# Kernel tuning notes

Measured on AMD Instinct MI355X. Metric: run time of the kernel, lower is better.

## Reference

```python
import jax, jax.numpy as jnp
import numpy as np

N_NODES = 50000
N_EDGES = 500000
N_REL = 8
D = 128        # input_dim
A_DIM = 64     # attention_dim
D_OUT = 128    # output_dim


def setup_inputs() -> dict:
    key = jax.random.key(0)
    ks = jax.random.split(key, 10)
    h = jax.random.normal(ks[0], (N_NODES, D), jnp.float32)
    # relation gate tables: [R, 2*D, D]; first D rows act on dst (subject), last D on src (object)
    relations = jax.random.normal(ks[1], (N_REL, 2 * D, D), jnp.float32) * 0.05
    rel_attention = jax.random.normal(ks[2], (N_REL, A_DIM), jnp.float32) * 0.05
    W_a = jax.random.normal(ks[3], (A_DIM, 2 * D), jnp.float32) * 0.05
    b_a = jnp.zeros((A_DIM,), jnp.float32)
    W_lin = jax.random.normal(ks[4], (D_OUT, 2 * D), jnp.float32) * 0.05
    b_lin = jnp.zeros((D_OUT,), jnp.float32)
    src = jax.random.randint(ks[5], (N_EDGES,), 0, N_NODES, dtype=jnp.int32)
    dst = jax.random.randint(ks[6], (N_EDGES,), 0, N_NODES, dtype=jnp.int32)
    etype = jax.random.randint(ks[7], (N_EDGES,), 0, N_REL, dtype=jnp.int32)
    return {"h": h, "relations": relations, "rel_attention": rel_attention,
            "W_a": W_a, "b_a": b_a, "W_lin": W_lin, "b_lin": b_lin,
            "src": src, "dst": dst, "etype": etype}


def reference(h, relations, rel_attention, W_a, b_a, W_lin, b_lin, src, dst, etype):
    d = h.shape[-1]
    # --- gates: relation-indexed gather_mm (concat gate type) ---
    # Project every node through every relation once (R is small), then gather per edge.
    proj_dst = jnp.einsum('nd,rde->rne', h, relations[:, :d, :])   # [R, N, D] subject/dst side
    proj_src = jnp.einsum('nd,rde->rne', h, relations[:, d:, :])   # [R, N, D] object/src side
    gate = jax.nn.sigmoid(proj_dst[etype, dst] + proj_src[etype, src])  # [E, D]

    src_h = h[src]   # [E, D]
    dst_h = h[dst]   # [E, D]

    # --- gatv2 attention (predicates are zeroed in the module -> rel_attention[0]) ---
    a = jax.nn.leaky_relu(jnp.concatenate([dst_h, src_h], axis=-1) @ W_a.T + b_a)  # [E, A]
    score = (rel_attention[0] * a).sum(-1)  # [E]

    # --- edge_softmax over destination-node segments ---
    smax = jax.ops.segment_max(score, dst, num_segments=N_NODES)
    ex = jnp.exp(score - smax[dst])
    denom = jax.ops.segment_sum(ex, dst, num_segments=N_NODES)
    attn = ex / denom[dst]  # [E]

    # --- message = u_mul_e(h, attn*gate), reduce = sum over dst ---
    msg = src_h * (attn[:, None] * gate)                 # [E, D]
    h_N = jax.ops.segment_sum(msg, dst, num_segments=N_NODES)  # [N, D]

    # --- graphsage aggregate: LeakyReLU(W [h ; h_N] + b) ---
    out = jax.nn.leaky_relu(jnp.concatenate([h, h_N], axis=-1) @ W_lin.T + b_lin)
    return out
```

## Files before the change

### kernel.cpp

```cpp
#include <hip/hip_runtime.h>
#include <cstdint>
#include <cstddef>

constexpr int NNODES = 50000;
constexpr int NEDGES = 500000;
constexpr int NRELS  = 8;
constexpr int DIM    = 128;
constexpr int ADIM   = 64;
constexpr int TWOD   = 256;
constexpr int EPB    = 64;
constexpr float SLOPE = 0.01f;

constexpr int XPITCH = TWOD + 8;
constexpr int SPAD = NEDGES + 1024;
constexpr int SCAN_CHUNK = 1000;
constexpr int NB_SCAN = NRELS * NNODES / SCAN_CHUNK;

typedef __attribute__((ext_vector_type(8))) short short8;
typedef __attribute__((ext_vector_type(4))) float floatx4;

__device__ __forceinline__ unsigned short f2bf(float f) {
    unsigned u = __float_as_uint(f);
    unsigned r = u + 0x7FFFu + ((u >> 16) & 1u);
    return (unsigned short)(r >> 16);
}
__device__ __forceinline__ float bf2f(unsigned short b) {
    return __uint_as_float(((unsigned)b) << 16);
}
__device__ __forceinline__ float sigmoid_fast(float x) {
    return __builtin_amdgcn_rcpf(1.0f + __expf(-x));
}

__global__ void k_init(int* __restrict__ histD, int* __restrict__ histRD,
                       int* __restrict__ cursorRD) {
    int i = blockIdx.x * blockDim.x + threadIdx.x;
    int stride = gridDim.x * blockDim.x;
    for (int idx = i; idx < NNODES; idx += stride) histD[idx] = 0;
    for (int idx = i; idx < NRELS * NNODES; idx += stride) {
        histRD[idx] = 0;
        cursorRD[idx] = 0;
    }
}

__global__ __launch_bounds__(256) void k_prep(const float* __restrict__ rel,
                                              const float* __restrict__ W_lin,
                                              const float* __restrict__ W_a,
                                              unsigned short* __restrict__ relT,
                                              unsigned short* __restrict__ Wl,
                                              unsigned short* __restrict__ Wa16) {
    __shared__ float ls[64][65];
    int b = blockIdx.x, t = threadIdx.x;
    if (b < 64) {
        int r = b >> 3, tile = b & 7;
        int d0 = (tile >> 1) * 64, o0 = (tile & 1) * 64;
        const float* rp = rel + ((size_t)r * TWOD + d0) * DIM + o0;
#pragma unroll
        for (int u = 0; u < 16; u++) {
            int v = u * 256 + t;
            int j = v & 63, i = v >> 6;
            ls[i][j] = rp[(size_t)i * DIM + j];
        }
        __syncthreads();
        unsigned short* wp = relT + ((size_t)r * DIM + o0) * TWOD + d0;
#pragma unroll
        for (int u = 0; u < 16; u++) {
            int v = u * 256 + t;
            int ii = v & 63, jj = v >> 6;
            wp[(size_t)jj * TWOD + ii] = f2bf(ls[ii][jj]);
        }
    } else {
        int idx = (b - 64) * 256 + t;
        if (idx < DIM * TWOD) {
            Wl[idx] = f2bf(W_lin[idx]);
        } else {
            int j = idx - DIM * TWOD;
            if (j < ADIM * TWOD) Wa16[j] = f2bf(W_a[j]);
        }
    }
}

__global__ void k_h16(const float* __restrict__ h, unsigned short* __restrict__ h16) {
    int i = blockIdx.x * 256 + threadIdx.x;
    if (i < NNODES * DIM / 8) {
        const float4* hp = (const float4*)(h + (size_t)i * 8);
        float4 a = hp[0], b = hp[1];
        union { unsigned short us[8]; short8 s8; } pk;
        pk.us[0] = f2bf(a.x); pk.us[1] = f2bf(a.y); pk.us[2] = f2bf(a.z); pk.us[3] = f2bf(a.w);
        pk.us[4] = f2bf(b.x); pk.us[5] = f2bf(b.y); pk.us[6] = f2bf(b.z); pk.us[7] = f2bf(b.w);
        *(short8*)&h16[(size_t)i * 8] = pk.s8;
    }
}

__global__ void k_hist2(const int* __restrict__ ety, const int* __restrict__ dst,
                        int* __restrict__ histRD, int* __restrict__ histD) {
    int e = blockIdx.x * 256 + threadIdx.x;
    if (e < NEDGES) {
        int r = ety[e], dn = dst[e];
        atomicAdd(&histRD[r * NNODES + dn], 1);
        atomicAdd(&histD[dn], 1);
    }
}

__global__ __launch_bounds__(256) void k_scanA(int* __restrict__ histRD,
                                               int* __restrict__ blockSums) {
    __shared__ int part[256];
    int b = blockIdx.x, t = threadIdx.x;
    int base = b * SCAN_CHUNK;
    int i0 = t * 4;
    int v[4]; int s = 0;
#pragma unroll
    for (int j = 0; j < 4; j++) {
        int i = i0 + j;
        v[j] = (i < SCAN_CHUNK) ? histRD[base + i] : 0;
        s += v[j];
    }
    part[t] = s;
    __syncthreads();
    for (int off = 1; off < 256; off <<= 1) {
        int x = (t >= off) ? part[t - off] : 0;
        __syncthreads();
        part[t] += x;
        __syncthreads();
    }
    int run = (t == 0) ? 0 : part[t - 1];
#pragma unroll
    for (int j = 0; j < 4; j++) {
        int i = i0 + j;
        if (i < SCAN_CHUNK) { histRD[base + i] = run; run += v[j]; }
    }
    if (t == 255) blockSums[b] = part[255];
}

__global__ __launch_bounds__(1024) void k_scanB(const int* __restrict__ blockSums,
                                                int* __restrict__ bp2,
                                                const int* __restrict__ histD,
                                                int* __restrict__ row_ptr,
                                                int* __restrict__ cursorD,
                                                int* __restrict__ offs,
                                                uint2* __restrict__ sMeta) {
    __shared__ int ls[1024];
    __shared__ int s_offs[NRELS + 1];
    __shared__ int s_cnt[NRELS];
    __shared__ int s_adj[NRELS];
    const int t = threadIdx.x;

    ls[t] = (t < NB_SCAN) ? blockSums[t] : 0;
    __syncthreads();
    for (int off = 1; off < 1024; off <<= 1) {
        int v = (t >= off) ? ls[t - off] : 0;
        __syncthreads();
        ls[t] += v;
        __syncthreads();
    }
    if (t == 0) {
        const int BPB = NNODES / SCAN_CHUNK;
        int off = 0;
        for (int r = 0; r < NRELS; r++) {
            int sf0 = (r == 0) ? 0 : ls[BPB * r - 1];
            int sf1 = ls[BPB * (r + 1) - 1];
            int cnt = sf1 - sf0;
            offs[r] = off; s_offs[r] = off; s_cnt[r] = cnt;
            s_adj[r] = off - sf0;
            off += ((cnt + EPB - 1) / EPB) * EPB;
        }
        s_offs[NRELS] = off;
    }
    __syncthreads();
    if (t < NB_SCAN) {
        int sf = (t == 0) ? 0 : ls[t - 1];
        bp2[t] = sf + s_adj[t / (NNODES / SCAN_CHUNK)];
    }
    __syncthreads();

    const int CH = (NNODES + 1023) / 1024;
    const int base = t * CH;
    int s = 0;
    for (int j = 0; j < CH; j++) { int i = base + j; if (i < NNODES) s += histD[i]; }
    ls[t] = s;
    __syncthreads();
    for (int off = 1; off < 1024; off <<= 1) {
        int v = (t >= off) ? ls[t - off] : 0;
        __syncthreads();
        ls[t] += v;
        __syncthreads();
    }
    int run = (t == 0) ? 0 : ls[t - 1];
    for (int j = 0; j < CH; j++) {
        int i = base + j;
        if (i < NNODES) { row_ptr[i] = run; cursorD[i] = 0; run += histD[i]; }
    }
    if (t == 1023) row_ptr[NNODES] = ls[1023];
    __syncthreads();

#pragma unroll
    for (int r = 0; r < NRELS; r++) {
        int s0 = s_offs[r] + s_cnt[r];
        int e0 = s_offs[r + 1];
        for (int idx = s0 + t; idx < e0; idx += 1024) sMeta[idx] = make_uint2(0xFFFFFFFFu, 0u);
    }
    for (int idx = s_offs[NRELS] + t; idx < SPAD; idx += 1024)
        sMeta[idx] = make_uint2(0xFFFFFFFFu, 0u);
}

__global__ void k_escatter(const int* __restrict__ ety, const int* __restrict__ src,
                           const int* __restrict__ dst, const int* __restrict__ row_ptr,
                           const int* __restrict__ histRD, const int* __restrict__ bp2,
                           int* __restrict__ cursorRD, int* __restrict__ cursorD,
                           uint2* __restrict__ sMeta) {
    int e = blockIdx.x * 256 + threadIdx.x;
    if (e >= NEDGES) return;
    int r = ety[e], sn = src[e], dn = dst[e];
    int idx = r * NNODES + dn;
    int rank = atomicAdd(&cursorRD[idx], 1);
    int slot = histRD[idx] + bp2[idx / SCAN_CHUNK] + rank;
    int pos = row_ptr[dn] + atomicAdd(&cursorD[dn], 1);
    sMeta[slot] = make_uint2((unsigned)sn | ((unsigned)dn << 16), (unsigned)pos);
}

__global__ __launch_bounds__(256, 4) void k_gate_msg(
    const unsigned short* __restrict__ h16, const unsigned short* __restrict__ relT,
    const unsigned short* __restrict__ Wa16,
    const uint2* __restrict__ sMeta, const float* __restrict__ b_a,
    const float* __restrict__ ratt, const int* __restrict__ offs,
    unsigned short* __restrict__ msgbuf, float* __restrict__ scoreP) {
    __shared__ unsigned short Xs[EPB * XPITCH];
    __shared__ int srcn_s[EPB];
    __shared__ int dstn_s[EPB];
    __shared__ int pos_s[EPB];
    __shared__ int val_s[EPB];
    __shared__ float scoreW[EPB][4];

    const int t = threadIdx.x;
    const int base = blockIdx.x * EPB;

    if (t < EPB) {
        uint2 m2 = sMeta[base + t];
        int valid = (m2.x != 0xFFFFFFFFu);
        val_s[t] = valid;
        srcn_s[t] = valid ? (int)(m2.x & 0xFFFFu) : 0;
        dstn_s[t] = valid ? (int)(m2.x >> 16) : 0;
        pos_s[t] = valid ? (int)m2.y : 0;
    }
    __syncthreads();
    if (!val_s[0]) return;

    int r = 0;
#pragma unroll
    for (int i = 1; i < NRELS; i++) if (base >= offs[i]) r = i;

#pragma unroll
    for (int u = 0; u < 8; u++) {
        int v = u * 256 + t;
        int i = v >> 5;
        int c = v & 31;
        int node = (c < 16) ? dstn_s[i] : srcn_s[i];
        *(short8*)&Xs[i * XPITCH + c * 8] = *(const short8*)&h16[(size_t)node * DIM + (c & 15) * 8];
    }

    const int wave = t >> 6;
    const int lane = t & 63;
    const int q = lane >> 4;
    const int l16 = lane & 15;
    const int o16 = wave * 16 + l16;

    const unsigned short* bp0 = relT + ((size_t)r * DIM + (wave * 2 + 0) * 16 + l16) * TWOD + q * 8;
    const unsigned short* bp1 = relT + ((size_t)r * DIM + (wave * 2 + 1) * 16 + l16) * TWOD + q * 8;
    const unsigned short* wb  = Wa16 + (size_t)o16 * TWOD + q * 8;

    short8 B0p[4], B1p[4], BSp[4];
#pragma unroll
    for (int ks = 0; ks < 4; ks++) {
        B0p[ks] = *(const short8*)(bp0 + ks * 32);
        B1p[ks] = *(const short8*)(bp1 + ks * 32);
        BSp[ks] = *(const short8*)(wb + ks * 32);
    }

    __syncthreads();

    floatx4 acc[4][2];
    floatx4 accS[4];
#pragma unroll
    for (int m = 0; m < 4; m++) {
        acc[m][0] = (floatx4)(0.0f);
        acc[m][1] = (floatx4)(0.0f);
        accS[m] = (floatx4)(0.0f);
    }

#pragma unroll
    for (int ks = 0; ks < 8; ks++) {
        short8 B0 = (ks < 4) ? B0p[ks & 3] : *(const short8*)(bp0 + ks * 32);
        short8 B1 = (ks < 4) ? B1p[ks & 3] : *(const short8*)(bp1 + ks * 32);
        short8 BS = (ks < 4) ? BSp[ks & 3] : *(const short8*)(wb + ks * 32);
        short8 Af[4];
        const unsigned short* xb = &Xs[l16 * XPITCH + ks * 32 + q * 8];
#pragma unroll
        for (int m = 0; m < 4; m++) Af[m] = *(const short8*)(xb + m * 16 * XPITCH);
#pragma unroll
        for (int m = 0; m < 4; m++) {
            acc[m][0] = __builtin_amdgcn_mfma_f32_16x16x32_bf16(Af[m], B0, acc[m][0], 0, 0, 0);
            acc[m][1] = __builtin_amdgcn_mfma_f32_16x16x32_bf16(Af[m], B1, acc[m][1], 0, 0, 0);
            accS[m]   = __builtin_amdgcn_mfma_f32_16x16x32_bf16(Af[m], BS, accS[m], 0, 0, 0);
        }
    }

    __syncthreads();

    {
        float ba = b_a[o16];
        float ra = ratt[o16];
#pragma unroll
        for (int m = 0; m < 4; m++) {
#pragma unroll
            for (int rg = 0; rg < 4; rg++) {
                float v = accS[m][rg] + ba;
                v = v > 0.0f ? v : SLOPE * v;
                v *= ra;
#pragma unroll
                for (int off = 8; off > 0; off >>= 1) v += __shfl_xor(v, off, 16);
                if (l16 == 0) scoreW[m * 16 + q * 4 + rg][wave] = v;
            }
        }
    }

#pragma unroll
    for (int m = 0; m < 4; m++) {
        int ib = m * 16 + q * 4;
#pragma unroll
        for (int nn = 0; nn < 2; nn++) {
            int o = (wave * 2 + nn) * 16 + l16;
#pragma unroll
            for (int rg = 0; rg < 4; rg++) {
                int i = ib + rg;
                float g = sigmoid_fast(acc[m][nn][rg]);
                float sh = bf2f(Xs[i * XPITCH + DIM + o]);
                Xs[i * XPITCH + o] = f2bf(sh * g);
            }
        }
    }
    __syncthreads();

#pragma unroll
    for (int u = 0; u < 4; u++) {
        int v = u * 256 + t;
        int i = v >> 4;
        int c = v & 15;
        if (!val_s[i]) continue;
        short8 val = *(const short8*)&Xs[i * XPITCH + c * 8];
        *(short8*)&msgbuf[(size_t)pos_s[i] * DIM + c * 8] = val;
    }
    if (t < EPB && val_s[t]) {
        scoreP[pos_s[t]] = scoreW[t][0] + scoreW[t][1] + scoreW[t][2] + scoreW[t][3];
    }
}

__global__ __launch_bounds__(256) void k_aggr(const unsigned short* __restrict__ msgbuf,
                                              const float* __restrict__ scoreP,
                                              const int* __restrict__ row_ptr,
                                              unsigned short* __restrict__ hN16) {
    int n = blockIdx.x * 4 + (threadIdx.x >> 6);
    int lane = threadIdx.x & 63;
    if (n >= NNODES) return;
    int p0 = row_ptr[n], p1 = row_ptr[n + 1];
    float a0 = 0.0f, a1 = 0.0f;
    if (p0 < p1) {
        float mx = -3.0e38f;
        for (int p = p0 + lane; p < p1; p += 64) mx = fmaxf(mx, scoreP[p]);
#pragma unroll
        for (int off = 32; off > 0; off >>= 1) mx = fmaxf(mx, __shfl_xor(mx, off));
        float sum = 0.0f;
        for (int p = p0 + lane; p < p1; p += 64) sum += __expf(scoreP[p] - mx);
#pragma unroll
        for (int off = 32; off > 0; off >>= 1) sum += __shfl_xor(sum, off);
        int p = p0;
        const unsigned short* mb = msgbuf + (size_t)lane * 2;
        for (; p + 4 <= p1; p += 4) {
            float w0 = __expf(scoreP[p + 0] - mx);
            float w1 = __expf(scoreP[p + 1] - mx);
            float w2 = __expf(scoreP[p + 2] - mx);
            float w3 = __expf(scoreP[p + 3] - mx);
            unsigned v0 = *(const unsigned*)&mb[(size_t)(p + 0) * DIM];
            unsigned v1 = *(const unsigned*)&mb[(size_t)(p + 1) * DIM];
            unsigned v2 = *(const unsigned*)&mb[(size_t)(p + 2) * DIM];
            unsigned v3 = *(const unsigned*)&mb[(size_t)(p + 3) * DIM];
            a0 = fmaf(w0, bf2f((unsigned short)(v0 & 0xFFFFu)), a0);
            a1 = fmaf(w0, bf2f((unsigned short)(v0 >> 16)), a1);
            a0 = fmaf(w1, bf2f((unsigned short)(v1 & 0xFFFFu)), a0);
            a1 = fmaf(w1, bf2f((unsigned short)(v1 >> 16)), a1);
            a0 = fmaf(w2, bf2f((unsigned short)(v2 & 0xFFFFu)), a0);
            a1 = fmaf(w2, bf2f((unsigned short)(v2 >> 16)), a1);
            a0 = fmaf(w3, bf2f((unsigned short)(v3 & 0xFFFFu)), a0);
            a1 = fmaf(w3, bf2f((unsigned short)(v3 >> 16)), a1);
        }
        for (; p < p1; p++) {
            float w = __expf(scoreP[p] - mx);
            unsigned v = *(const unsigned*)&mb[(size_t)p * DIM];
            a0 = fmaf(w, bf2f((unsigned short)(v & 0xFFFFu)), a0);
            a1 = fmaf(w, bf2f((unsigned short)(v >> 16)), a1);
        }
        float inv = __builtin_amdgcn_rcpf(sum);
        a0 *= inv; a1 *= inv;
    }
    unsigned o = (unsigned)f2bf(a0) | ((unsigned)f2bf(a1) << 16);
    *(unsigned*)&hN16[(size_t)n * DIM + lane * 2] = o;
}

__global__ __launch_bounds__(256) void k_out(const unsigned short* __restrict__ h16,
                                             const unsigned short* __restrict__ hN16,
                                             const unsigned short* __restrict__ Wl,
                                             const float* __restrict__ b_lin,
                                             float* __restrict__ out) {
    __shared__ unsigned short Xs[EPB * XPITCH];
    const int t = threadIdx.x;
    const int nb = blockIdx.x * 64;

#pragma unroll
    for (int u = 0; u < 8; u++) {
        int v = u * 256 + t;
        int i = v >> 5;
        int c = v & 31;
        int n = nb + i;
        if (n >= NNODES) n = NNODES - 1;
        const unsigned short* srcp = (c < 16) ? h16 : hN16;
        *(short8*)&Xs[i * XPITCH + c * 8] = *(const short8*)&srcp[(size_t)n * DIM + (c & 15) * 8];
    }

    const int wave = t >> 6;
    const int lane = t & 63;
    const int q = lane >> 4;
    const int l16 = lane & 15;

    short8 Bf[2][8];
#pragma unroll
    for (int nn = 0; nn < 2; nn++) {
        int o = (wave * 2 + nn) * 16 + l16;
        const unsigned short* bp = Wl + (size_t)o * TWOD + q * 8;
#pragma unroll
        for (int ks = 0; ks < 8; ks++) Bf[nn][ks] = *(const short8*)(bp + ks * 32);
    }

    __syncthreads();

    floatx4 acc[4][2];
#pragma unroll
    for (int m = 0; m < 4; m++)
#pragma unroll
        for (int nn = 0; nn < 2; nn++) acc[m][nn] = (floatx4)(0.0f);

#pragma unroll
    for (int ks = 0; ks < 8; ks++) {
        short8 Af[4];
        const unsigned short* xb = &Xs[l16 * XPITCH + ks * 32 + q * 8];
#pragma unroll
        for (int m = 0; m < 4; m++) Af[m] = *(const short8*)(xb + m * 16 * XPITCH);
#pragma unroll
        for (int m = 0; m < 4; m++)
#pragma unroll
            for (int nn = 0; nn < 2; nn++)
                acc[m][nn] = __builtin_amdgcn_mfma_f32_16x16x32_bf16(Af[m], Bf[nn][ks], acc[m][nn], 0, 0, 0);
    }

#pragma unroll
    for (int m = 0; m < 4; m++) {
        int ib = m * 16 + q * 4;
#pragma unroll
        for (int nn = 0; nn < 2; nn++) {
            int o = (wave * 2 + nn) * 16 + l16;
            float bl = b_lin[o];
#pragma unroll
            for (int rg = 0; rg < 4; rg++) {
                int n = nb + ib + rg;
                if (n < NNODES) {
                    float val = acc[m][nn][rg] + bl;
                    val = val > 0.0f ? val : SLOPE * val;
                    out[(size_t)n * DIM + o] = val;
                }
            }
        }
    }
}

extern "C" void kernel_launch(void* const* d_in, const int* in_sizes, int n_in,
                              void* d_out, int out_size, void* d_ws, size_t ws_size,
                              hipStream_t stream) {
    const float* h     = (const float*)d_in[0];
    const float* rel   = (const float*)d_in[1];
    const float* ratt  = (const float*)d_in[2];
    const float* W_a   = (const float*)d_in[3];
    const float* b_a   = (const float*)d_in[4];
    const float* W_lin = (const float*)d_in[5];
    const float* b_lin = (const float*)d_in[6];
    const int* src = (const int*)d_in[7];
    const int* dst = (const int*)d_in[8];
    const int* ety = (const int*)d_in[9];
    float* out = (float*)d_out;

    float* scoreP = (float*)d_ws;
    unsigned short* h16  = (unsigned short*)(scoreP + NEDGES);
    unsigned short* hN16 = h16 + (size_t)NNODES * DIM;
    unsigned short* relT = hN16 + (size_t)NNODES * DIM;
    unsigned short* Wl   = relT + (size_t)NRELS * DIM * TWOD;
    unsigned short* Wa16 = Wl + (size_t)DIM * TWOD;
    uint2* sMeta = (uint2*)(Wa16 + (size_t)ADIM * TWOD);
    int* row_ptr = (int*)(sMeta + SPAD);
    int* histD   = row_ptr + (NNODES + 1);
    int* cursorD = histD + NNODES;
    int* cnts    = cursorD + NNODES;
    int* offs    = cnts + 16;
    unsigned short* msgbuf = (unsigned short*)(((uintptr_t)(offs + 8) + 255) & ~(uintptr_t)255);
    int* histRD    = (int*)msgbuf;
    int* cursorRD  = histRD + NRELS * NNODES;
    int* blockSums = cursorRD + NRELS * NNODES;
    int* bp2       = blockSums + 512;

    k_init<<<1024, 256, 0, stream>>>(histD, histRD, cursorRD);
    k_prep<<<64 + (DIM * TWOD + ADIM * TWOD + 255) / 256, 256, 0, stream>>>(
        rel, W_lin, W_a, relT, Wl, Wa16);
    k_h16<<<(NNODES * DIM / 8 + 255) / 256, 256, 0, stream>>>(h, h16);
    k_hist2<<<(NEDGES + 255) / 256, 256, 0, stream>>>(ety, dst, histRD, histD);
    k_scanA<<<NB_SCAN, 256, 0, stream>>>(histRD, blockSums);
    k_scanB<<<1, 1024, 0, stream>>>(blockSums, bp2, histD, row_ptr, cursorD, offs, sMeta);
    k_escatter<<<(NEDGES + 255) / 256, 256, 0, stream>>>(
        ety, src, dst, row_ptr, histRD, bp2, cursorRD, cursorD, sMeta);
    k_gate_msg<<<(NEDGES + 8 * EPB + EPB - 1) / EPB, 256, 0, stream>>>(
        h16, relT, Wa16, sMeta, b_a, ratt, offs, msgbuf, scoreP);
    k_aggr<<<(NNODES + 3) / 4, 256, 0, stream>>>(msgbuf, scoreP, row_ptr, hN16);
    k_out<<<(NNODES + 63) / 64, 256, 0, stream>>>(h16, hN16, Wl, b_lin, out);
}
```

Before: 490.2 us.

## Process two edge groups per block with register-prefetched gathers; fold cursor reset into scan

```diff
diff --git a/kernel.cpp b/kernel.cpp
--- a/kernel.cpp
+++ b/kernel.cpp
@@ -15,6 +15,7 @@
 constexpr int SPAD = NEDGES + 1024;
 constexpr int SCAN_CHUNK = 1000;
 constexpr int NB_SCAN = NRELS * NNODES / SCAN_CHUNK;
+constexpr int NGRP = (NEDGES + 8 * EPB + EPB - 1) / EPB;
 
 typedef __attribute__((ext_vector_type(8))) short short8;
 typedef __attribute__((ext_vector_type(4))) float floatx4;
@@ -30,16 +31,16 @@
 __device__ __forceinline__ float sigmoid_fast(float x) {
     return __builtin_amdgcn_rcpf(1.0f + __expf(-x));
 }
-
-__global__ void k_init(int* __restrict__ histD, int* __restrict__ histRD,
-                       int* __restrict__ cursorRD) {
+__device__ __forceinline__ void barrier_lgkm() {
+    asm volatile("s_waitcnt lgkmcnt(0)" ::: "memory");
+    __builtin_amdgcn_s_barrier();
+}
+
+__global__ void k_init(int* __restrict__ histD, int* __restrict__ histRD) {
     int i = blockIdx.x * blockDim.x + threadIdx.x;
     int stride = gridDim.x * blockDim.x;
     for (int idx = i; idx < NNODES; idx += stride) histD[idx] = 0;
-    for (int idx = i; idx < NRELS * NNODES; idx += stride) {
-        histRD[idx] = 0;
-        cursorRD[idx] = 0;
-    }
+    for (int idx = i; idx < NRELS * NNODES; idx += stride) histRD[idx] = 0;
 }
 
 __global__ __launch_bounds__(256) void k_prep(const float* __restrict__ rel,
@@ -102,7 +103,8 @@
 }
 
 __global__ __launch_bounds__(256) void k_scanA(int* __restrict__ histRD,
-                                               int* __restrict__ blockSums) {
+                                               int* __restrict__ blockSums,
+                                               int* __restrict__ cursorRD) {
     __shared__ int part[256];
     int b = blockIdx.x, t = threadIdx.x;
     int base = b * SCAN_CHUNK;
@@ -126,7 +128,7 @@
 #pragma unroll
     for (int j = 0; j < 4; j++) {
         int i = i0 + j;
-        if (i < SCAN_CHUNK) { histRD[base + i] = run; run += v[j]; }
+        if (i < SCAN_CHUNK) { histRD[base + i] = run; cursorRD[base + i] = 0; run += v[j]; }
     }
     if (t == 255) blockSums[b] = part[255];
 }
@@ -224,37 +226,46 @@
     const float* __restrict__ ratt, const int* __restrict__ offs,
     unsigned short* __restrict__ msgbuf, float* __restrict__ scoreP) {
     __shared__ unsigned short Xs[EPB * XPITCH];
-    __shared__ int srcn_s[EPB];
-    __shared__ int dstn_s[EPB];
-    __shared__ int pos_s[EPB];
-    __shared__ int val_s[EPB];
+    __shared__ int srcn_s[2][EPB];
+    __shared__ int dstn_s[2][EPB];
+    __shared__ int pos_s[2][EPB];
+    __shared__ int val_s[2][EPB];
     __shared__ float scoreW[EPB][4];
 
     const int t = threadIdx.x;
-    const int base = blockIdx.x * EPB;
+    const int g0 = blockIdx.x * 2;
 
     if (t < EPB) {
-        uint2 m2 = sMeta[base + t];
+        uint2 m2 = sMeta[(size_t)g0 * EPB + t];
         int valid = (m2.x != 0xFFFFFFFFu);
-        val_s[t] = valid;
-        srcn_s[t] = valid ? (int)(m2.x & 0xFFFFu) : 0;
-        dstn_s[t] = valid ? (int)(m2.x >> 16) : 0;
-        pos_s[t] = valid ? (int)m2.y : 0;
-    }
-    __syncthreads();
-    if (!val_s[0]) return;
-
-    int r = 0;
-#pragma unroll
-    for (int i = 1; i < NRELS; i++) if (base >= offs[i]) r = i;
-
+        val_s[0][t] = valid;
+        srcn_s[0][t] = valid ? (int)(m2.x & 0xFFFFu) : 0;
+        dstn_s[0][t] = valid ? (int)(m2.x >> 16) : 0;
+        pos_s[0][t] = valid ? (int)m2.y : 0;
+        int v1 = 0;
+        if (g0 + 1 < NGRP) {
+            uint2 m3 = sMeta[(size_t)(g0 + 1) * EPB + t];
+            v1 = (m3.x != 0xFFFFFFFFu);
+            srcn_s[1][t] = v1 ? (int)(m3.x & 0xFFFFu) : 0;
+            dstn_s[1][t] = v1 ? (int)(m3.x >> 16) : 0;
+            pos_s[1][t] = v1 ? (int)m3.y : 0;
+        }
+        val_s[1][t] = v1;
+    }
+    __syncthreads();
+    if (!val_s[0][0]) return;
+    const int ng = val_s[1][0] ? 2 : 1;
+
+    const int i0 = t >> 5;
+    const int c  = t & 31;
+    const int ch = (c & 15) * 8;
+
+    short8 G[8];
 #pragma unroll
     for (int u = 0; u < 8; u++) {
-        int v = u * 256 + t;
-        int i = v >> 5;
-        int c = v & 31;
-        int node = (c < 16) ? dstn_s[i] : srcn_s[i];
-        *(short8*)&Xs[i * XPITCH + c * 8] = *(const short8*)&h16[(size_t)node * DIM + (c & 15) * 8];
+        int i = u * 8 + i0;
+        int node = (c < 16) ? dstn_s[0][i] : srcn_s[0][i];
+        G[u] = *(const short8*)&h16[(size_t)node * DIM + ch];
     }
 
     const int wave = t >> 6;
@@ -262,52 +273,74 @@
     const int q = lane >> 4;
     const int l16 = lane & 15;
     const int o16 = wave * 16 + l16;
-
-    const unsigned short* bp0 = relT + ((size_t)r * DIM + (wave * 2 + 0) * 16 + l16) * TWOD + q * 8;
-    const unsigned short* bp1 = relT + ((size_t)r * DIM + (wave * 2 + 1) * 16 + l16) * TWOD + q * 8;
-    const unsigned short* wb  = Wa16 + (size_t)o16 * TWOD + q * 8;
-
-    short8 B0p[4], B1p[4], BSp[4];
-#pragma unroll
-    for (int ks = 0; ks < 4; ks++) {
-        B0p[ks] = *(const short8*)(bp0 + ks * 32);
-        B1p[ks] = *(const short8*)(bp1 + ks * 32);
-        BSp[ks] = *(const short8*)(wb + ks * 32);
-    }
-
-    __syncthreads();
-
-    floatx4 acc[4][2];
-    floatx4 accS[4];
-#pragma unroll
-    for (int m = 0; m < 4; m++) {
-        acc[m][0] = (floatx4)(0.0f);
-        acc[m][1] = (floatx4)(0.0f);
-        accS[m] = (floatx4)(0.0f);
-    }
-
-#pragma unroll
-    for (int ks = 0; ks < 8; ks++) {
-        short8 B0 = (ks < 4) ? B0p[ks & 3] : *(const short8*)(bp0 + ks * 32);
-        short8 B1 = (ks < 4) ? B1p[ks & 3] : *(const short8*)(bp1 + ks * 32);
-        short8 BS = (ks < 4) ? BSp[ks & 3] : *(const short8*)(wb + ks * 32);
-        short8 Af[4];
-        const unsigned short* xb = &Xs[l16 * XPITCH + ks * 32 + q * 8];
-#pragma unroll
-        for (int m = 0; m < 4; m++) Af[m] = *(const short8*)(xb + m * 16 * XPITCH);
+    const float ba = b_a[o16];
+    const float ra = ratt[o16];
+
+    for (int gi = 0; gi < ng; gi++) {
+        const int base = (g0 + gi) * EPB;
+
+#pragma unroll
+        for (int u = 0; u < 8; u++) {
+            int i = u * 8 + i0;
+            *(short8*)&Xs[i * XPITCH + c * 8] = G[u];
+        }
+
+        if (gi + 1 < ng) {
+#pragma unroll
+            for (int u = 0; u < 8; u++) {
+                int i = u * 8 + i0;
+                int node = (c < 16) ? dstn_s[1][i] : srcn_s[1][i];
+                G[u] = *(const short8*)&h16[(size_t)node * DIM + ch];
+            }
+            __builtin_amdgcn_sched_barrier(0);
+        }
+
+        int r = 0;
+#pragma unroll
+        for (int i = 1; i < NRELS; i++) if (base >= offs[i]) r = i;
+
+        const unsigned short* bp0 = relT + ((size_t)r * DIM + (wave * 2 + 0) * 16 + l16) * TWOD + q * 8;
+        const unsigned short* bp1 = relT + ((size_t)r * DIM + (wave * 2 + 1) * 16 + l16) * TWOD + q * 8;
+        const unsigned short* wb  = Wa16 + (size_t)o16 * TWOD + q * 8;
+
+        short8 B0p[4], B1p[4], BSp[4];
+#pragma unroll
+        for (int ks = 0; ks < 4; ks++) {
+            B0p[ks] = *(const short8*)(bp0 + ks * 32);
+            B1p[ks] = *(const short8*)(bp1 + ks * 32);
+            BSp[ks] = *(const short8*)(wb + ks * 32);
+        }
+
+        barrier_lgkm();
+
+        floatx4 acc[4][2];
+        floatx4 accS[4];
 #pragma unroll
         for (int m = 0; m < 4; m++) {
-            acc[m][0] = __builtin_amdgcn_mfma_f32_16x16x32_bf16(Af[m], B0, acc[m][0], 0, 0, 0);
-            acc[m][1] = __builtin_amdgcn_mfma_f32_16x16x32_bf16(Af[m], B1, acc[m][1], 0, 0, 0);
-            accS[m]   = __builtin_amdgcn_mfma_f32_16x16x32_bf16(Af[m], BS, accS[m], 0, 0, 0);
-        }
-    }
-
-    __syncthreads();
-
-    {
-        float ba = b_a[o16];
-        float ra = ratt[o16];
+            acc[m][0] = (floatx4)(0.0f);
+            acc[m][1] = (floatx4)(0.0f);
+            accS[m] = (floatx4)(0.0f);
+        }
+
+#pragma unroll
+        for (int ks = 0; ks < 8; ks++) {
+            short8 B0 = (ks < 4) ? B0p[ks & 3] : *(const short8*)(bp0 + ks * 32);
+            short8 B1 = (ks < 4) ? B1p[ks & 3] : *(const short8*)(bp1 + ks * 32);
+            short8 BS = (ks < 4) ? BSp[ks & 3] : *(const short8*)(wb + ks * 32);
+            short8 Af[4];
+            const unsigned short* xb = &Xs[l16 * XPITCH + ks * 32 + q * 8];
+#pragma unroll
+            for (int m = 0; m < 4; m++) Af[m] = *(const short8*)(xb + m * 16 * XPITCH);
+#pragma unroll
+            for (int m = 0; m < 4; m++) {
+                acc[m][0] = __builtin_amdgcn_mfma_f32_16x16x32_bf16(Af[m], B0, acc[m][0], 0, 0, 0);
+                acc[m][1] = __builtin_amdgcn_mfma_f32_16x16x32_bf16(Af[m], B1, acc[m][1], 0, 0, 0);
+                accS[m]   = __builtin_amdgcn_mfma_f32_16x16x32_bf16(Af[m], BS, accS[m], 0, 0, 0);
+            }
+        }
+
+        barrier_lgkm();
+
 #pragma unroll
         for (int m = 0; m < 4; m++) {
 #pragma unroll
@@ -320,36 +353,39 @@
                 if (l16 == 0) scoreW[m * 16 + q * 4 + rg][wave] = v;
             }
         }
-    }
-
-#pragma unroll
-    for (int m = 0; m < 4; m++) {
-        int ib = m * 16 + q * 4;
-#pragma unroll
-        for (int nn = 0; nn < 2; nn++) {
-            int o = (wave * 2 + nn) * 16 + l16;
-#pragma unroll
-            for (int rg = 0; rg < 4; rg++) {
-                int i = ib + rg;
-                float g = sigmoid_fast(acc[m][nn][rg]);
-                float sh = bf2f(Xs[i * XPITCH + DIM + o]);
-                Xs[i * XPITCH + o] = f2bf(sh * g);
+
+#pragma unroll
+        for (int m = 0; m < 4; m++) {
+            int ib = m * 16 + q * 4;
+#pragma unroll
+            for (int nn = 0; nn < 2; nn++) {
+                int o = (wave * 2 + nn) * 16 + l16;
+#pragma unroll
+                for (int rg = 0; rg < 4; rg++) {
+                    int i = ib + rg;
+                    float g = sigmoid_fast(acc[m][nn][rg]);
+                    float sh = bf2f(Xs[i * XPITCH + DIM + o]);
+                    Xs[i * XPITCH + o] = f2bf(sh * g);
+                }
             }
         }
-    }
-    __syncthreads();
-
-#pragma unroll
-    for (int u = 0; u < 4; u++) {
-        int v = u * 256 + t;
-        int i = v >> 4;
-        int c = v & 15;
-        if (!val_s[i]) continue;
-        short8 val = *(const short8*)&Xs[i * XPITCH + c * 8];
-        *(short8*)&msgbuf[(size_t)pos_s[i] * DIM + c * 8] = val;
-    }
-    if (t < EPB && val_s[t]) {
-        scoreP[pos_s[t]] = scoreW[t][0] + scoreW[t][1] + scoreW[t][2] + scoreW[t][3];
+        barrier_lgkm();
+
+#pragma unroll
+        for (int u = 0; u < 4; u++) {
+            int v = u * 256 + t;
+            int i = v >> 4;
+            int cc = v & 15;
+            if (val_s[gi][i]) {
+                short8 val = *(const short8*)&Xs[i * XPITCH + cc * 8];
+                *(short8*)&msgbuf[(size_t)pos_s[gi][i] * DIM + cc * 8] = val;
+            }
+        }
+        if (t < EPB && val_s[gi][t]) {
+            scoreP[pos_s[gi][t]] = scoreW[t][0] + scoreW[t][1] + scoreW[t][2] + scoreW[t][3];
+        }
+
+        if (gi + 1 < ng) barrier_lgkm();
     }
 }
 
@@ -512,16 +548,16 @@
     int* blockSums = cursorRD + NRELS * NNODES;
     int* bp2       = blockSums + 512;
 
-    k_init<<<1024, 256, 0, stream>>>(histD, histRD, cursorRD);
+    k_init<<<1024, 256, 0, stream>>>(histD, histRD);
     k_prep<<<64 + (DIM * TWOD + ADIM * TWOD + 255) / 256, 256, 0, stream>>>(
         rel, W_lin, W_a, relT, Wl, Wa16);
     k_h16<<<(NNODES * DIM / 8 + 255) / 256, 256, 0, stream>>>(h, h16);
     k_hist2<<<(NEDGES + 255) / 256, 256, 0, stream>>>(ety, dst, histRD, histD);
-    k_scanA<<<NB_SCAN, 256, 0, stream>>>(histRD, blockSums);
+    k_scanA<<<NB_SCAN, 256, 0, stream>>>(histRD, blockSums, cursorRD);
     k_scanB<<<1, 1024, 0, stream>>>(blockSums, bp2, histD, row_ptr, cursorD, offs, sMeta);
     k_escatter<<<(NEDGES + 255) / 256, 256, 0, stream>>>(
         ety, src, dst, row_ptr, histRD, bp2, cursorRD, cursorD, sMeta);
-    k_gate_msg<<<(NEDGES + 8 * EPB + EPB - 1) / EPB, 256, 0, stream>>>(
+    k_gate_msg<<<(NGRP + 1) / 2, 256, 0, stream>>>(
         h16, relT, Wa16, sMeta, b_a, ratt, offs, msgbuf, scoreP);
     k_aggr<<<(NNODES + 3) / 4, 256, 0, stream>>>(msgbuf, scoreP, row_ptr, hN16);
     k_out<<<(NNODES + 63) / 64, 256, 0, stream>>>(h16, hN16, Wl, b_lin, out);
```

Result: slower. 573.3 us (+16.9%).
